# Optimization experiments

Hardware: AMD Instinct MI355X
Metric: run time of the kernel (lower is better)

The kernel has to match this reference:

```python
import jax, jax.numpy as jnp
import numpy as np


def setup_inputs() -> dict:
    key = jax.random.key(0)
    k1, k2, k3, k4 = jax.random.split(key, 4)
    B, S, D, Y = 8, 2048, 512, 8921
    # xavier_uniform scale for [Y, D] weights
    lim = float(np.sqrt(6.0 / (Y + D)))
    x = jax.random.normal(k1, (B, S, D), dtype=jnp.float32)
    U_w = jax.random.uniform(k2, (Y, D), minval=-lim, maxval=lim, dtype=jnp.float32)
    final_w = jax.random.uniform(k3, (Y, D), minval=-lim, maxval=lim, dtype=jnp.float32)
    final_b = jax.random.normal(k4, (Y,), dtype=jnp.float32) * 0.02
    return {"x": x, "U_w": U_w, "final_w": final_w, "final_b": final_b}


def reference(x, U_w, final_w, final_b):
    # att: [B, Y, S] = U_w @ x^T
    att = jnp.einsum("yd,bsd->bys", U_w, x)
    alpha = jax.nn.softmax(att, axis=2)          # softmax over sequence
    m = jnp.einsum("bys,bsd->byd", alpha, x)      # per-label context [B, Y, D]
    y = jnp.einsum("yd,byd->by", final_w, m) + final_b  # [B, Y]
    return y
```

## Files before the change

### kernel.cpp

```cpp
#include <hip/hip_runtime.h>
#include <hip/hip_bf16.h>

constexpr int B_ = 8;
constexpr int S_ = 2048;
constexpr int D_ = 512;
constexpr int Y_ = 8921;
constexpr int MT_ = 70;
constexpr int SG_ = 4;

typedef __attribute__((ext_vector_type(8))) __bf16 bf16x8;
typedef __attribute__((ext_vector_type(4))) float f32x4;

__device__ __forceinline__ int swz_el(int row, int ksel8) {
  return row * 64 + ((ksel8 ^ row) & 7) * 8;
}

__global__ __launch_bounds__(256) void cvtW(const float* __restrict__ U,
                                            const float* __restrict__ F,
                                            __hip_bfloat16* __restrict__ wsW) {
  const int c = blockIdx.x * 256 + threadIdx.x;
  const int tile = c >> 11;
  const int row = (c >> 3) & 255;
  const int cs = c & 7;
  const int mt = tile >> 3, kt = tile & 7;
  const int ch = cs ^ (row & 7);
  const int g = row >> 5, h = (row >> 4) & 1, w = row & 15;
  const int y = mt * 128 + g * 16 + w;
  float4 f0 = {0.f, 0.f, 0.f, 0.f}, f1 = {0.f, 0.f, 0.f, 0.f};
  if (y < Y_) {
    const float* src = (h ? F : U) + (size_t)y * D_ + kt * 64 + ch * 8;
    f0 = reinterpret_cast<const float4*>(src)[0];
    f1 = reinterpret_cast<const float4*>(src)[1];
  }
  bf16x8 v;
  v[0] = (__bf16)f0.x; v[1] = (__bf16)f0.y; v[2] = (__bf16)f0.z; v[3] = (__bf16)f0.w;
  v[4] = (__bf16)f1.x; v[5] = (__bf16)f1.y; v[6] = (__bf16)f1.z; v[7] = (__bf16)f1.w;
  *reinterpret_cast<bf16x8*>(wsW + (size_t)c * 8) = v;
}

__global__ __launch_bounds__(256) void cvtX(const float* __restrict__ x,
                                            __hip_bfloat16* __restrict__ wsX) {
  const int c = blockIdx.x * 256 + threadIdx.x;
  const int tile = c >> 11;
  const int row = (c >> 3) & 255;
  const int cs = c & 7;
  const int b = tile >> 6, st = (tile >> 3) & 7, kt = tile & 7;
  const int ch = cs ^ (row & 7);
  const int s = st * 256 + row;
  const float* src = x + ((size_t)b * S_ + s) * D_ + kt * 64 + ch * 8;
  const float4 f0 = reinterpret_cast<const float4*>(src)[0];
  const float4 f1 = reinterpret_cast<const float4*>(src)[1];
  bf16x8 v;
  v[0] = (__bf16)f0.x; v[1] = (__bf16)f0.y; v[2] = (__bf16)f0.z; v[3] = (__bf16)f0.w;
  v[4] = (__bf16)f1.x; v[5] = (__bf16)f1.y; v[6] = (__bf16)f1.z; v[7] = (__bf16)f1.w;
  *reinterpret_cast<bf16x8*>(wsX + (size_t)c * 8) = v;
}

__global__ __launch_bounds__(256) void zeroLN(float* __restrict__ LN, int n) {
  const int i = blockIdx.x * 256 + threadIdx.x;
  if (i < n) LN[i] = 0.f;
}

__global__ __launch_bounds__(256) void combine(const float* __restrict__ Lg,
                                               const float* __restrict__ Ng,
                                               const float* __restrict__ fb,
                                               float* __restrict__ out) {
  const int y = blockIdx.x * 256 + threadIdx.x;
  const int b = blockIdx.y;
  if (y < Y_) out[(size_t)b * Y_ + y] = Ng[b * Y_ + y] / Lg[b * Y_ + y] + fb[y];
}

typedef const __attribute__((address_space(1))) void gv_t;
typedef __attribute__((address_space(3))) void lv_t;

__device__ __forceinline__ void gld_lds16(const void* g, void* l) {
  __builtin_amdgcn_global_load_lds((gv_t*)g, (lv_t*)l, 16, 0, 0);
}

__global__ __launch_bounds__(512, 2) void pool_main(
    const __hip_bfloat16* __restrict__ wsW, const __hip_bfloat16* __restrict__ wsX,
    float* __restrict__ Lg, float* __restrict__ Ng) {
  const int bid = blockIdx.x;
  const int b = bid & 7;
  const int r = bid >> 3;
  const int mt = r % MT_;
  const int sg = r / MT_;

  const int tid = threadIdx.x;
  const int lane = tid & 63;
  const int wid = tid >> 6;
  const int wm = wid >> 2;
  const int wn = wid & 3;
  const int l15 = lane & 15;
  const int l4 = lane >> 4;

  extern __shared__ __bf16 ldsA[];
  float* redL = reinterpret_cast<float*>(ldsA + 65536);
  float* redN = redL + 128;

  if (tid < 256) redL[tid] = 0.f;

  const __bf16* Wbase = (const __bf16*)wsW + (size_t)mt * 8 * 16384;
  const __bf16* Xbase = (const __bf16*)wsX + ((size_t)(b * 8 + sg * 2) * 8) * 16384;

  f32x4 acc[8][4];

  auto stageBoth = [&](int t1) {
    const int par = t1 & 1;
    const char* srcW = (const char*)(Wbase + (t1 & 7) * 16384) + wid * 4096 + lane * 16;
    const char* srcX = (const char*)(Xbase + (size_t)t1 * 16384) + wid * 4096 + lane * 16;
    char* dstW = (char*)ldsA + par * 32768 + wid * 4096;
    char* dstX = (char*)ldsA + 65536 + par * 32768 + wid * 4096;
#pragma unroll
    for (int i = 0; i < 4; ++i) gld_lds16(srcW + i * 1024, dstW + i * 1024);
#pragma unroll
    for (int i = 0; i < 4; ++i) gld_lds16(srcX + i * 1024, dstX + i * 1024);
  };

  auto fold = [&]() {
#pragma unroll
    for (int g = 0; g < 4; ++g)
#pragma unroll
      for (int q = 0; q < 4; ++q) {
        float l = 0.f, nn = 0.f;
#pragma unroll
        for (int n = 0; n < 4; ++n) {
          const float e = __expf(acc[2 * g][n][q]);
          l += e;
          nn = fmaf(e, acc[2 * g + 1][n][q], nn);
        }
#pragma unroll
        for (int mask = 1; mask <= 8; mask <<= 1) {
          l += __shfl_xor(l, mask);
          nn += __shfl_xor(nn, mask);
        }
        if (l15 == 0) {
          const int yl = wm * 64 + g * 16 + (l4 << 2) + q;
          atomicAdd(&redL[yl], l);
          atomicAdd(&redN[yl], nn);
        }
      }
  };

  auto zacc = [&]() {
#pragma unroll
    for (int m = 0; m < 8; ++m)
#pragma unroll
      for (int n = 0; n < 4; ++n) acc[m][n] = (f32x4){0.f, 0.f, 0.f, 0.f};
  };

  stageBoth(0);
  zacc();

  for (int t = 0; t < 16; ++t) {
    __syncthreads();
    if (t < 15) stageBoth(t + 1);

    const __bf16* A = ldsA + ((t & 1) << 14);
    const __bf16* Xl = ldsA + 32768 + ((t & 1) << 14);

    {
      bf16x8 xf[4], af[8];
#pragma unroll
      for (int n = 0; n < 4; ++n)
        xf[n] = *reinterpret_cast<const bf16x8*>(&Xl[swz_el(wn * 64 + n * 16 + l15, l4)]);
#pragma unroll
      for (int j = 0; j < 8; ++j)
        af[j] = *reinterpret_cast<const bf16x8*>(&A[swz_el(wm * 128 + j * 16 + l15, l4)]);
      __builtin_amdgcn_s_setprio(1);
#pragma unroll
      for (int j = 0; j < 8; ++j)
#pragma unroll
        for (int n = 0; n < 4; ++n)
          acc[j][n] = __builtin_amdgcn_mfma_f32_16x16x32_bf16(af[j], xf[n], acc[j][n], 0, 0, 0);
      __builtin_amdgcn_s_setprio(0);
    }
    {
      bf16x8 xf[4], af[8];
#pragma unroll
      for (int n = 0; n < 4; ++n)
        xf[n] = *reinterpret_cast<const bf16x8*>(&Xl[swz_el(wn * 64 + n * 16 + l15, 4 + l4)]);
#pragma unroll
      for (int j = 0; j < 8; ++j)
        af[j] = *reinterpret_cast<const bf16x8*>(&A[swz_el(wm * 128 + j * 16 + l15, 4 + l4)]);
      __builtin_amdgcn_s_setprio(1);
#pragma unroll
      for (int j = 0; j < 8; ++j)
#pragma unroll
        for (int n = 0; n < 4; ++n)
          acc[j][n] = __builtin_amdgcn_mfma_f32_16x16x32_bf16(af[j], xf[n], acc[j][n], 0, 0, 0);
      __builtin_amdgcn_s_setprio(0);
    }

    if (t == 7) { fold(); zacc(); }
  }
  fold();

  __syncthreads();
  if (tid < 128) {
    const int y = mt * 128 + tid;
    if (y < Y_) {
      atomicAdd(&Lg[(size_t)b * Y_ + y], redL[tid]);
      atomicAdd(&Ng[(size_t)b * Y_ + y], redN[tid]);
    }
  }
}

constexpr int FB_BY = 128, FB_BS = 64, FB_BK = 64;

__device__ __forceinline__ int fswz(int row, int k) {
  return row * FB_BK + ((((k >> 3) ^ row) & 7) << 3) + (k & 7);
}

template <int CHUNKS>
__device__ __forceinline__ void fb_stage(const float* __restrict__ gbase, int rstride,
                                         int maxrow, __bf16* lds, int tid) {
#pragma unroll
  for (int i = 0; i < CHUNKS / 256; ++i) {
    const int c = tid + 256 * i;
    const int row = c >> 3;
    const int ch = c & 7;
    float4 f0 = {0.f, 0.f, 0.f, 0.f}, f1 = {0.f, 0.f, 0.f, 0.f};
    if (row < maxrow) {
      const float4* p = reinterpret_cast<const float4*>(gbase + (size_t)row * rstride + ch * 8);
      f0 = p[0]; f1 = p[1];
    }
    bf16x8 v;
    v[0] = (__bf16)f0.x; v[1] = (__bf16)f0.y; v[2] = (__bf16)f0.z; v[3] = (__bf16)f0.w;
    v[4] = (__bf16)f1.x; v[5] = (__bf16)f1.y; v[6] = (__bf16)f1.z; v[7] = (__bf16)f1.w;
    *reinterpret_cast<bf16x8*>(&lds[fswz(row, ch * 8)]) = v;
  }
}

__global__ __launch_bounds__(256) void output_layer_fallback(
    const float* __restrict__ x, const float* __restrict__ Uw,
    const float* __restrict__ Fw, const float* __restrict__ fb,
    float* __restrict__ out) {
  const int b = blockIdx.y;
  const int y0 = blockIdx.x * FB_BY;
  const int tid = threadIdx.x;
  const int lane = tid & 63;
  const int w = tid >> 6;
  const int wm = (w >> 1) * 64, wn = (w & 1) * 32;
  __shared__ __bf16 sU[FB_BY * FB_BK], sF[FB_BY * FB_BK], sX[FB_BS * FB_BK];
  float Ls[4][4], Ns[4][4];
#pragma unroll
  for (int m = 0; m < 4; ++m)
#pragma unroll
    for (int q = 0; q < 4; ++q) { Ls[m][q] = 0.f; Ns[m][q] = 0.f; }
  const float* xb = x + (size_t)b * S_ * D_;
  const int umax = Y_ - y0;
  for (int s0 = 0; s0 < S_; s0 += FB_BS) {
    f32x4 accA[4][2] = {}, accP[4][2] = {};
    for (int k0 = 0; k0 < D_; k0 += FB_BK) {
      __syncthreads();
      fb_stage<FB_BY * 8>(Uw + (size_t)y0 * D_ + k0, D_, umax, sU, tid);
      fb_stage<FB_BY * 8>(Fw + (size_t)y0 * D_ + k0, D_, umax, sF, tid);
      fb_stage<FB_BS * 8>(xb + (size_t)s0 * D_ + k0, D_, FB_BS, sX, tid);
      __syncthreads();
#pragma unroll
      for (int kk = 0; kk < 2; ++kk) {
        const int kb = kk * 32 + (lane >> 4) * 8;
        bf16x8 bx[2];
#pragma unroll
        for (int n = 0; n < 2; ++n)
          bx[n] = *reinterpret_cast<const bf16x8*>(&sX[fswz(wn + n * 16 + (lane & 15), kb)]);
#pragma unroll
        for (int m = 0; m < 4; ++m) {
          const bf16x8 aU = *reinterpret_cast<const bf16x8*>(&sU[fswz(wm + m * 16 + (lane & 15), kb)]);
          const bf16x8 aF = *reinterpret_cast<const bf16x8*>(&sF[fswz(wm + m * 16 + (lane & 15), kb)]);
#pragma unroll
          for (int n = 0; n < 2; ++n) {
            accA[m][n] = __builtin_amdgcn_mfma_f32_16x16x32_bf16(aU, bx[n], accA[m][n], 0, 0, 0);
            accP[m][n] = __builtin_amdgcn_mfma_f32_16x16x32_bf16(aF, bx[n], accP[m][n], 0, 0, 0);
          }
        }
      }
    }
#pragma unroll
    for (int m = 0; m < 4; ++m)
#pragma unroll
      for (int n = 0; n < 2; ++n)
#pragma unroll
        for (int q = 0; q < 4; ++q) {
          const float e = __expf(accA[m][n][q]);
          Ls[m][q] += e;
          Ns[m][q] = fmaf(e, accP[m][n][q], Ns[m][q]);
        }
  }
  __syncthreads();
  float* redL = reinterpret_cast<float*>(sU);
  float* redN = reinterpret_cast<float*>(sF);
  for (int i = tid; i < FB_BY; i += 256) { redL[i] = 0.f; redN[i] = 0.f; }
  __syncthreads();
#pragma unroll
  for (int m = 0; m < 4; ++m)
#pragma unroll
    for (int q = 0; q < 4; ++q) {
      float l = Ls[m][q], nn = Ns[m][q];
#pragma unroll
      for (int mask = 1; mask <= 8; mask <<= 1) {
        l += __shfl_xor(l, mask);
        nn += __shfl_xor(nn, mask);
      }
      if ((lane & 15) == 0) {
        const int yl = wm + m * 16 + ((lane >> 4) << 2) + q;
        atomicAdd(&redL[yl], l);
        atomicAdd(&redN[yl], nn);
      }
    }
  __syncthreads();
  for (int i = tid; i < FB_BY; i += 256) {
    const int y = y0 + i;
    if (y < Y_) out[(size_t)b * Y_ + y] = redN[i] / redL[i] + fb[y];
  }
}

extern "C" void kernel_launch(void* const* d_in, const int* in_sizes, int n_in,
                              void* d_out, int out_size, void* d_ws,
                              size_t ws_size, hipStream_t stream) {
  const float* x = (const float*)d_in[0];
  const float* Uw = (const float*)d_in[1];
  const float* Fw = (const float*)d_in[2];
  const float* fb = (const float*)d_in[3];
  float* out = (float*)d_out;

  constexpr size_t W_EL = (size_t)MT_ * 8 * 16384;
  constexpr size_t X_EL = (size_t)B_ * 64 * 16384;
  constexpr size_t LN_FL = (size_t)2 * B_ * Y_;
  constexpr size_t WS_NEED = (W_EL + X_EL) * 2 + LN_FL * 4;
  constexpr int LDS_BYTES = 4 * 32768 + 1024;

  if (ws_size >= WS_NEED) {
    __hip_bfloat16* wsW = (__hip_bfloat16*)d_ws;
    __hip_bfloat16* wsX = wsW + W_EL;
    float* Lg = (float*)(wsX + X_EL);
    float* Ng = Lg + (size_t)B_ * Y_;

    cvtW<<<dim3((unsigned)(W_EL / 8 / 256)), dim3(256), 0, stream>>>(Uw, Fw, wsW);
    cvtX<<<dim3((unsigned)(X_EL / 8 / 256)), dim3(256), 0, stream>>>(x, wsX);
    zeroLN<<<dim3((unsigned)((LN_FL + 255) / 256)), dim3(256), 0, stream>>>(Lg, (int)LN_FL);

    hipFuncSetAttribute((const void*)pool_main,
                        hipFuncAttributeMaxDynamicSharedMemorySize, LDS_BYTES);
    pool_main<<<dim3(MT_ * B_ * SG_), dim3(512), LDS_BYTES, stream>>>(wsW, wsX, Lg, Ng);
    combine<<<dim3((Y_ + 255) / 256, B_), dim3(256), 0, stream>>>(Lg, Ng, fb, out);
  } else {
    output_layer_fallback<<<dim3(MT_, B_), dim3(256), 0, stream>>>(x, Uw, Fw, fb, out);
  }
}
```

Before: 347.6 us.

## Shrink pool_main tiles to 64 labels x 256 seq with K=32 steps

Retiles the fused attention-pooling kernel: each block now covers 64 labels (32 U rows plus 32 final rows) by 256 sequence positions, with 16 K-steps of 32. Workspace layouts and swizzles in the conversion kernels change to match. LDS use drops to static buffers so more blocks fit per CU, and the launch bound asks for 4 blocks. The cost is that each x tile is reloaded twice as often across label tiles, and there are more global atomics because there are more sequence groups.

```diff
diff --git a/kernel.cpp b/kernel.cpp
--- a/kernel.cpp
+++ b/kernel.cpp
@@ -5,30 +5,30 @@
 constexpr int S_ = 2048;
 constexpr int D_ = 512;
 constexpr int Y_ = 8921;
-constexpr int MT_ = 70;
-constexpr int SG_ = 4;
+constexpr int MT_ = 140;
+constexpr int SG_ = 8;
 
 typedef __attribute__((ext_vector_type(8))) __bf16 bf16x8;
 typedef __attribute__((ext_vector_type(4))) float f32x4;
 
-__device__ __forceinline__ int swz_el(int row, int ksel8) {
-  return row * 64 + ((ksel8 ^ row) & 7) * 8;
+__device__ __forceinline__ int swz32(int row, int ksel) {
+  return row * 32 + (((ksel ^ (row >> 1)) & 3) << 3);
 }
 
 __global__ __launch_bounds__(256) void cvtW(const float* __restrict__ U,
                                             const float* __restrict__ F,
                                             __hip_bfloat16* __restrict__ wsW) {
   const int c = blockIdx.x * 256 + threadIdx.x;
-  const int tile = c >> 11;
-  const int row = (c >> 3) & 255;
-  const int cs = c & 7;
-  const int mt = tile >> 3, kt = tile & 7;
-  const int ch = cs ^ (row & 7);
+  const int tile = c >> 9;
+  const int row = (c >> 2) & 127;
+  const int cs = c & 3;
+  const int mt = tile >> 4, kt = tile & 15;
+  const int ch = (cs ^ (row >> 1)) & 3;
   const int g = row >> 5, h = (row >> 4) & 1, w = row & 15;
-  const int y = mt * 128 + g * 16 + w;
+  const int y = mt * 64 + g * 16 + w;
   float4 f0 = {0.f, 0.f, 0.f, 0.f}, f1 = {0.f, 0.f, 0.f, 0.f};
   if (y < Y_) {
-    const float* src = (h ? F : U) + (size_t)y * D_ + kt * 64 + ch * 8;
+    const float* src = (h ? F : U) + (size_t)y * D_ + kt * 32 + ch * 8;
     f0 = reinterpret_cast<const float4*>(src)[0];
     f1 = reinterpret_cast<const float4*>(src)[1];
   }
@@ -41,13 +41,13 @@
 __global__ __launch_bounds__(256) void cvtX(const float* __restrict__ x,
                                             __hip_bfloat16* __restrict__ wsX) {
   const int c = blockIdx.x * 256 + threadIdx.x;
-  const int tile = c >> 11;
-  const int row = (c >> 3) & 255;
-  const int cs = c & 7;
-  const int b = tile >> 6, st = (tile >> 3) & 7, kt = tile & 7;
-  const int ch = cs ^ (row & 7);
+  const int tile = c >> 10;
+  const int row = (c >> 2) & 255;
+  const int cs = c & 3;
+  const int b = tile >> 7, st = (tile >> 4) & 7, kt = tile & 15;
+  const int ch = (cs ^ (row >> 1)) & 3;
   const int s = st * 256 + row;
-  const float* src = x + ((size_t)b * S_ + s) * D_ + kt * 64 + ch * 8;
+  const float* src = x + ((size_t)b * S_ + s) * D_ + kt * 32 + ch * 8;
   const float4 f0 = reinterpret_cast<const float4*>(src)[0];
   const float4 f1 = reinterpret_cast<const float4*>(src)[1];
   bf16x8 v;
@@ -77,7 +77,7 @@
   __builtin_amdgcn_global_load_lds((gv_t*)g, (lv_t*)l, 16, 0, 0);
 }
 
-__global__ __launch_bounds__(512, 2) void pool_main(
+__global__ __launch_bounds__(512, 4) void pool_main(
     const __hip_bfloat16* __restrict__ wsW, const __hip_bfloat16* __restrict__ wsX,
     float* __restrict__ Lg, float* __restrict__ Ng) {
   const int bid = blockIdx.x;
@@ -94,114 +94,84 @@
   const int l15 = lane & 15;
   const int l4 = lane >> 4;
 
-  extern __shared__ __bf16 ldsA[];
-  float* redL = reinterpret_cast<float*>(ldsA + 65536);
-  float* redN = redL + 128;
-
-  if (tid < 256) redL[tid] = 0.f;
-
-  const __bf16* Wbase = (const __bf16*)wsW + (size_t)mt * 8 * 16384;
-  const __bf16* Xbase = (const __bf16*)wsX + ((size_t)(b * 8 + sg * 2) * 8) * 16384;
-
-  f32x4 acc[8][4];
+  __shared__ __bf16 sW[2][4096];
+  __shared__ __bf16 sX[2][8192];
+  __shared__ float red[128];
+
+  if (tid < 128) red[tid] = 0.f;
+
+  const __bf16* Wbase = (const __bf16*)wsW + (size_t)mt * 16 * 4096;
+  const __bf16* Xbase = (const __bf16*)wsX + (size_t)((b * 8 + sg) * 16) * 8192;
+
+  f32x4 acc[4][4];
+#pragma unroll
+  for (int m = 0; m < 4; ++m)
+#pragma unroll
+    for (int n = 0; n < 4; ++n) acc[m][n] = (f32x4){0.f, 0.f, 0.f, 0.f};
 
   auto stageBoth = [&](int t1) {
     const int par = t1 & 1;
-    const char* srcW = (const char*)(Wbase + (t1 & 7) * 16384) + wid * 4096 + lane * 16;
-    const char* srcX = (const char*)(Xbase + (size_t)t1 * 16384) + wid * 4096 + lane * 16;
-    char* dstW = (char*)ldsA + par * 32768 + wid * 4096;
-    char* dstX = (char*)ldsA + 65536 + par * 32768 + wid * 4096;
-#pragma unroll
-    for (int i = 0; i < 4; ++i) gld_lds16(srcW + i * 1024, dstW + i * 1024);
-#pragma unroll
-    for (int i = 0; i < 4; ++i) gld_lds16(srcX + i * 1024, dstX + i * 1024);
+    const char* srcW = (const char*)(Wbase + t1 * 4096) + tid * 16;
+    const char* srcX = (const char*)(Xbase + (size_t)t1 * 8192) + tid * 16;
+    gld_lds16(srcW, (char*)sW[par] + tid * 16);
+    gld_lds16(srcX, (char*)sX[par] + tid * 16);
+    gld_lds16(srcX + 8192, (char*)sX[par] + 8192 + tid * 16);
   };
 
-  auto fold = [&]() {
-#pragma unroll
-    for (int g = 0; g < 4; ++g)
-#pragma unroll
-      for (int q = 0; q < 4; ++q) {
-        float l = 0.f, nn = 0.f;
-#pragma unroll
-        for (int n = 0; n < 4; ++n) {
-          const float e = __expf(acc[2 * g][n][q]);
-          l += e;
-          nn = fmaf(e, acc[2 * g + 1][n][q], nn);
-        }
-#pragma unroll
-        for (int mask = 1; mask <= 8; mask <<= 1) {
-          l += __shfl_xor(l, mask);
-          nn += __shfl_xor(nn, mask);
-        }
-        if (l15 == 0) {
-          const int yl = wm * 64 + g * 16 + (l4 << 2) + q;
-          atomicAdd(&redL[yl], l);
-          atomicAdd(&redN[yl], nn);
-        }
-      }
-  };
-
-  auto zacc = [&]() {
-#pragma unroll
-    for (int m = 0; m < 8; ++m)
-#pragma unroll
-      for (int n = 0; n < 4; ++n) acc[m][n] = (f32x4){0.f, 0.f, 0.f, 0.f};
-  };
-
   stageBoth(0);
-  zacc();
 
   for (int t = 0; t < 16; ++t) {
     __syncthreads();
     if (t < 15) stageBoth(t + 1);
 
-    const __bf16* A = ldsA + ((t & 1) << 14);
-    const __bf16* Xl = ldsA + 32768 + ((t & 1) << 14);
-
-    {
-      bf16x8 xf[4], af[8];
+    const __bf16* A = sW[t & 1];
+    const __bf16* Xl = sX[t & 1];
+
+    bf16x8 af[4], xf[4];
+#pragma unroll
+    for (int j = 0; j < 4; ++j)
+      af[j] = *reinterpret_cast<const bf16x8*>(&A[swz32(wm * 64 + j * 16 + l15, l4)]);
+#pragma unroll
+    for (int n = 0; n < 4; ++n)
+      xf[n] = *reinterpret_cast<const bf16x8*>(&Xl[swz32(wn * 64 + n * 16 + l15, l4)]);
+    __builtin_amdgcn_s_setprio(1);
+#pragma unroll
+    for (int j = 0; j < 4; ++j)
 #pragma unroll
       for (int n = 0; n < 4; ++n)
-        xf[n] = *reinterpret_cast<const bf16x8*>(&Xl[swz_el(wn * 64 + n * 16 + l15, l4)]);
-#pragma unroll
-      for (int j = 0; j < 8; ++j)
-        af[j] = *reinterpret_cast<const bf16x8*>(&A[swz_el(wm * 128 + j * 16 + l15, l4)]);
-      __builtin_amdgcn_s_setprio(1);
-#pragma unroll
-      for (int j = 0; j < 8; ++j)
-#pragma unroll
-        for (int n = 0; n < 4; ++n)
-          acc[j][n] = __builtin_amdgcn_mfma_f32_16x16x32_bf16(af[j], xf[n], acc[j][n], 0, 0, 0);
-      __builtin_amdgcn_s_setprio(0);
-    }
-    {
-      bf16x8 xf[4], af[8];
-#pragma unroll
-      for (int n = 0; n < 4; ++n)
-        xf[n] = *reinterpret_cast<const bf16x8*>(&Xl[swz_el(wn * 64 + n * 16 + l15, 4 + l4)]);
-#pragma unroll
-      for (int j = 0; j < 8; ++j)
-        af[j] = *reinterpret_cast<const bf16x8*>(&A[swz_el(wm * 128 + j * 16 + l15, 4 + l4)]);
-      __builtin_amdgcn_s_setprio(1);
-#pragma unroll
-      for (int j = 0; j < 8; ++j)
-#pragma unroll
-        for (int n = 0; n < 4; ++n)
-          acc[j][n] = __builtin_amdgcn_mfma_f32_16x16x32_bf16(af[j], xf[n], acc[j][n], 0, 0, 0);
-      __builtin_amdgcn_s_setprio(0);
-    }
-
-    if (t == 7) { fold(); zacc(); }
-  }
-  fold();
+        acc[j][n] = __builtin_amdgcn_mfma_f32_16x16x32_bf16(af[j], xf[n], acc[j][n], 0, 0, 0);
+    __builtin_amdgcn_s_setprio(0);
+  }
+
+#pragma unroll
+  for (int g = 0; g < 2; ++g)
+#pragma unroll
+    for (int q = 0; q < 4; ++q) {
+      float l = 0.f, nn = 0.f;
+#pragma unroll
+      for (int n = 0; n < 4; ++n) {
+        const float e = __expf(acc[2 * g][n][q]);
+        l += e;
+        nn = fmaf(e, acc[2 * g + 1][n][q], nn);
+      }
+#pragma unroll
+      for (int mask = 1; mask <= 8; mask <<= 1) {
+        l += __shfl_xor(l, mask);
+        nn += __shfl_xor(nn, mask);
+      }
+      if (l15 == 0) {
+        const int yl = wm * 32 + g * 16 + (l4 << 2) + q;
+        atomicAdd(&red[yl], l);
+        atomicAdd(&red[64 + yl], nn);
+      }
+    }
 
   __syncthreads();
-  if (tid < 128) {
-    const int y = mt * 128 + tid;
+  if (tid < 64) {
+    const int y = mt * 64 + tid;
     if (y < Y_) {
-      atomicAdd(&Lg[(size_t)b * Y_ + y], redL[tid]);
-      atomicAdd(&Ng[(size_t)b * Y_ + y], redN[tid]);
+      atomicAdd(&Lg[(size_t)b * Y_ + y], red[tid]);
+      atomicAdd(&Ng[(size_t)b * Y_ + y], red[64 + tid]);
     }
   }
 }
@@ -325,11 +295,10 @@
   const float* fb = (const float*)d_in[3];
   float* out = (float*)d_out;
 
-  constexpr size_t W_EL = (size_t)MT_ * 8 * 16384;
-  constexpr size_t X_EL = (size_t)B_ * 64 * 16384;
+  constexpr size_t W_EL = (size_t)MT_ * 16 * 4096;
+  constexpr size_t X_EL = (size_t)B_ * 8 * 16 * 8192;
   constexpr size_t LN_FL = (size_t)2 * B_ * Y_;
   constexpr size_t WS_NEED = (W_EL + X_EL) * 2 + LN_FL * 4;
-  constexpr int LDS_BYTES = 4 * 32768 + 1024;
 
   if (ws_size >= WS_NEED) {
     __hip_bfloat16* wsW = (__hip_bfloat16*)d_ws;
@@ -341,11 +310,9 @@
     cvtX<<<dim3((unsigned)(X_EL / 8 / 256)), dim3(256), 0, stream>>>(x, wsX);
     zeroLN<<<dim3((unsigned)((LN_FL + 255) / 256)), dim3(256), 0, stream>>>(Lg, (int)LN_FL);
 
-    hipFuncSetAttribute((const void*)pool_main,
-                        hipFuncAttributeMaxDynamicSharedMemorySize, LDS_BYTES);
-    pool_main<<<dim3(MT_ * B_ * SG_), dim3(512), LDS_BYTES, stream>>>(wsW, wsX, Lg, Ng);
+    pool_main<<<dim3(MT_ * B_ * SG_), dim3(512), 0, stream>>>(wsW, wsX, Lg, Ng);
     combine<<<dim3((Y_ + 255) / 256, B_), dim3(256), 0, stream>>>(Lg, Ng, fb, out);
   } else {
-    output_layer_fallback<<<dim3(MT_, B_), dim3(256), 0, stream>>>(x, Uw, Fw, fb, out);
-  }
-}
+    output_layer_fallback<<<dim3(MT_ / 2 + 5, B_), dim3(256), 0, stream>>>(x, Uw, Fw, fb, out);
+  }
+}
```

Measured after the change: 344.7 us. No clear change (-0.8%).

## Triple-buffer K=32 tiles with split W/X staging and explicit vmcnt waits

Applied to the files above, without the earlier changes.

Halves the K-tile depth from 64 to 32 and changes the bf16 workspace layout and swizzle to match. pool_main now keeps three LDS buffers, prefetches two steps ahead, and splits W and X staging across the two half-steps, using s_waitcnt vmcnt and raw s_barriers instead of __syncthreads. The aim is to overlap global-to-LDS loads with MFMA work more fully and to cut LDS use so more blocks can be resident per CU. In exchange there are twice as many loop iterations and barriers, and the hand-placed vmcnt counts must stay correct or tiles will be read before their loads finish.

```diff
diff --git a/kernel.cpp b/kernel.cpp
--- a/kernel.cpp
+++ b/kernel.cpp
@@ -11,24 +11,24 @@
 typedef __attribute__((ext_vector_type(8))) __bf16 bf16x8;
 typedef __attribute__((ext_vector_type(4))) float f32x4;
 
-__device__ __forceinline__ int swz_el(int row, int ksel8) {
-  return row * 64 + ((ksel8 ^ row) & 7) * 8;
+__device__ __forceinline__ int swz32(int row, int ksel) {
+  return row * 32 + (((ksel ^ (row >> 1)) & 3) << 3);
 }
 
 __global__ __launch_bounds__(256) void cvtW(const float* __restrict__ U,
                                             const float* __restrict__ F,
                                             __hip_bfloat16* __restrict__ wsW) {
   const int c = blockIdx.x * 256 + threadIdx.x;
-  const int tile = c >> 11;
-  const int row = (c >> 3) & 255;
-  const int cs = c & 7;
-  const int mt = tile >> 3, kt = tile & 7;
-  const int ch = cs ^ (row & 7);
+  const int tile = c >> 10;
+  const int row = (c >> 2) & 255;
+  const int cs = c & 3;
+  const int mt = tile >> 4, kt = tile & 15;
+  const int ch = (cs ^ (row >> 1)) & 3;
   const int g = row >> 5, h = (row >> 4) & 1, w = row & 15;
   const int y = mt * 128 + g * 16 + w;
   float4 f0 = {0.f, 0.f, 0.f, 0.f}, f1 = {0.f, 0.f, 0.f, 0.f};
   if (y < Y_) {
-    const float* src = (h ? F : U) + (size_t)y * D_ + kt * 64 + ch * 8;
+    const float* src = (h ? F : U) + (size_t)y * D_ + kt * 32 + ch * 8;
     f0 = reinterpret_cast<const float4*>(src)[0];
     f1 = reinterpret_cast<const float4*>(src)[1];
   }
@@ -41,13 +41,13 @@
 __global__ __launch_bounds__(256) void cvtX(const float* __restrict__ x,
                                             __hip_bfloat16* __restrict__ wsX) {
   const int c = blockIdx.x * 256 + threadIdx.x;
-  const int tile = c >> 11;
-  const int row = (c >> 3) & 255;
-  const int cs = c & 7;
-  const int b = tile >> 6, st = (tile >> 3) & 7, kt = tile & 7;
-  const int ch = cs ^ (row & 7);
+  const int tile = c >> 10;
+  const int row = (c >> 2) & 255;
+  const int cs = c & 3;
+  const int b = tile >> 7, st = (tile >> 4) & 7, kt = tile & 15;
+  const int ch = (cs ^ (row >> 1)) & 3;
   const int s = st * 256 + row;
-  const float* src = x + ((size_t)b * S_ + s) * D_ + kt * 64 + ch * 8;
+  const float* src = x + ((size_t)b * S_ + s) * D_ + kt * 32 + ch * 8;
   const float4 f0 = reinterpret_cast<const float4*>(src)[0];
   const float4 f1 = reinterpret_cast<const float4*>(src)[1];
   bf16x8 v;
@@ -95,26 +95,31 @@
   const int l4 = lane >> 4;
 
   extern __shared__ __bf16 ldsA[];
-  float* redL = reinterpret_cast<float*>(ldsA + 65536);
+  float* redL = reinterpret_cast<float*>(ldsA + 49152);
   float* redN = redL + 128;
 
   if (tid < 256) redL[tid] = 0.f;
 
-  const __bf16* Wbase = (const __bf16*)wsW + (size_t)mt * 8 * 16384;
-  const __bf16* Xbase = (const __bf16*)wsX + ((size_t)(b * 8 + sg * 2) * 8) * 16384;
+  const __bf16* Wbase = (const __bf16*)wsW + (size_t)mt * 16 * 8192;
+  const __bf16* Xbase = (const __bf16*)wsX + (size_t)((b * 8 + sg * 2) * 16) * 8192;
 
   f32x4 acc[8][4];
-
-  auto stageBoth = [&](int t1) {
-    const int par = t1 & 1;
-    const char* srcW = (const char*)(Wbase + (t1 & 7) * 16384) + wid * 4096 + lane * 16;
-    const char* srcX = (const char*)(Xbase + (size_t)t1 * 16384) + wid * 4096 + lane * 16;
-    char* dstW = (char*)ldsA + par * 32768 + wid * 4096;
-    char* dstX = (char*)ldsA + 65536 + par * 32768 + wid * 4096;
-#pragma unroll
-    for (int i = 0; i < 4; ++i) gld_lds16(srcW + i * 1024, dstW + i * 1024);
-#pragma unroll
-    for (int i = 0; i < 4; ++i) gld_lds16(srcX + i * 1024, dstX + i * 1024);
+#pragma unroll
+  for (int m = 0; m < 8; ++m)
+#pragma unroll
+    for (int n = 0; n < 4; ++n) acc[m][n] = (f32x4){0.f, 0.f, 0.f, 0.f};
+
+  auto stageW = [&](int t1, int buf) {
+    const char* src = (const char*)(Wbase + (size_t)(t1 & 15) * 8192) + tid * 16;
+    char* dst = (char*)(ldsA + buf * 8192) + tid * 16;
+    gld_lds16(src, dst);
+    gld_lds16(src + 8192, dst + 8192);
+  };
+  auto stageX = [&](int t1, int buf) {
+    const char* src = (const char*)(Xbase + (size_t)t1 * 8192) + tid * 16;
+    char* dst = (char*)(ldsA + 24576 + buf * 8192) + tid * 16;
+    gld_lds16(src, dst);
+    gld_lds16(src + 8192, dst + 8192);
   };
 
   auto fold = [&]() {
@@ -149,50 +154,63 @@
       for (int n = 0; n < 4; ++n) acc[m][n] = (f32x4){0.f, 0.f, 0.f, 0.f};
   };
 
-  stageBoth(0);
-  zacc();
-
-  for (int t = 0; t < 16; ++t) {
-    __syncthreads();
-    if (t < 15) stageBoth(t + 1);
-
-    const __bf16* A = ldsA + ((t & 1) << 14);
-    const __bf16* Xl = ldsA + 32768 + ((t & 1) << 14);
-
+  stageW(0, 0); stageX(0, 0);
+  stageW(1, 1); stageX(1, 1);
+  asm volatile("s_waitcnt vmcnt(4)" ::: "memory");
+  __builtin_amdgcn_s_barrier();
+  __builtin_amdgcn_sched_barrier(0);
+
+  int cur = 0;
+  int nx2 = 2;
+
+  for (int t = 0; t < 32; ++t) {
+    const __bf16* A = ldsA + cur * 8192;
+    const __bf16* Xl = ldsA + 24576 + cur * 8192;
+    const bool pre = (t < 30);
+
+    bf16x8 xf[4];
     {
-      bf16x8 xf[4], af[8];
+      bf16x8 af[4];
+#pragma unroll
+      for (int j = 0; j < 4; ++j)
+        af[j] = *reinterpret_cast<const bf16x8*>(&A[swz32(wm * 128 + j * 16 + l15, l4)]);
 #pragma unroll
       for (int n = 0; n < 4; ++n)
-        xf[n] = *reinterpret_cast<const bf16x8*>(&Xl[swz_el(wn * 64 + n * 16 + l15, l4)]);
-#pragma unroll
-      for (int j = 0; j < 8; ++j)
-        af[j] = *reinterpret_cast<const bf16x8*>(&A[swz_el(wm * 128 + j * 16 + l15, l4)]);
+        xf[n] = *reinterpret_cast<const bf16x8*>(&Xl[swz32(wn * 64 + n * 16 + l15, l4)]);
+      if (pre) stageW(t + 2, nx2);
+      __builtin_amdgcn_s_barrier();
       __builtin_amdgcn_s_setprio(1);
 #pragma unroll
-      for (int j = 0; j < 8; ++j)
+      for (int j = 0; j < 4; ++j)
 #pragma unroll
         for (int n = 0; n < 4; ++n)
           acc[j][n] = __builtin_amdgcn_mfma_f32_16x16x32_bf16(af[j], xf[n], acc[j][n], 0, 0, 0);
       __builtin_amdgcn_s_setprio(0);
+      __builtin_amdgcn_s_barrier();
     }
     {
-      bf16x8 xf[4], af[8];
-#pragma unroll
-      for (int n = 0; n < 4; ++n)
-        xf[n] = *reinterpret_cast<const bf16x8*>(&Xl[swz_el(wn * 64 + n * 16 + l15, 4 + l4)]);
-#pragma unroll
-      for (int j = 0; j < 8; ++j)
-        af[j] = *reinterpret_cast<const bf16x8*>(&A[swz_el(wm * 128 + j * 16 + l15, 4 + l4)]);
+      bf16x8 af[4];
+#pragma unroll
+      for (int j = 0; j < 4; ++j)
+        af[j] = *reinterpret_cast<const bf16x8*>(&A[swz32(wm * 128 + (4 + j) * 16 + l15, l4)]);
+      if (pre) stageX(t + 2, nx2);
+      __builtin_amdgcn_s_barrier();
       __builtin_amdgcn_s_setprio(1);
 #pragma unroll
-      for (int j = 0; j < 8; ++j)
+      for (int j = 0; j < 4; ++j)
 #pragma unroll
         for (int n = 0; n < 4; ++n)
-          acc[j][n] = __builtin_amdgcn_mfma_f32_16x16x32_bf16(af[j], xf[n], acc[j][n], 0, 0, 0);
+          acc[4 + j][n] = __builtin_amdgcn_mfma_f32_16x16x32_bf16(af[j], xf[n], acc[4 + j][n], 0, 0, 0);
       __builtin_amdgcn_s_setprio(0);
-    }
-
-    if (t == 7) { fold(); zacc(); }
+      if (t < 30) asm volatile("s_waitcnt vmcnt(4)" ::: "memory");
+      else if (t == 30) asm volatile("s_waitcnt vmcnt(0)" ::: "memory");
+      __builtin_amdgcn_s_barrier();
+      __builtin_amdgcn_sched_barrier(0);
+    }
+
+    if (t == 15) { fold(); zacc(); }
+    cur = (cur == 2) ? 0 : cur + 1;
+    nx2 = (nx2 == 2) ? 0 : nx2 + 1;
   }
   fold();
 
@@ -325,11 +343,11 @@
   const float* fb = (const float*)d_in[3];
   float* out = (float*)d_out;
 
-  constexpr size_t W_EL = (size_t)MT_ * 8 * 16384;
-  constexpr size_t X_EL = (size_t)B_ * 64 * 16384;
+  constexpr size_t W_EL = (size_t)MT_ * 16 * 8192;
+  constexpr size_t X_EL = (size_t)B_ * 8 * 16 * 8192;
   constexpr size_t LN_FL = (size_t)2 * B_ * Y_;
   constexpr size_t WS_NEED = (W_EL + X_EL) * 2 + LN_FL * 4;
-  constexpr int LDS_BYTES = 4 * 32768 + 1024;
+  constexpr int LDS_BYTES = 6 * 16384 + 1024;
 
   if (ws_size >= WS_NEED) {
     __hip_bfloat16* wsW = (__hip_bfloat16*)d_ws;
```

Result: slower. 368.1 us (+5.9%).
